# Kernel tuning notes

Measured on AMD Instinct MI355X. Metric: run time of the kernel, lower is better.

The kernel has to match this reference:

```python
import jax, jax.numpy as jnp
import numpy as np

# Config matching init_kwargs
D_MODEL = 1024   # input_size
D_HEAD = 2048    # head_size (expert hidden)
N_EXPERTS = 8
TOP_K = 2


def setup_inputs() -> dict:
    key = jax.random.key(0)
    k_x, k_g, k_w1, k_b1, k_w2, k_b2 = jax.random.split(key, 6)
    B, S = 4, 1024
    x = jax.random.normal(k_x, (B, S, D_MODEL), dtype=jnp.float32)
    # f_gate: nn.Linear(input_size, num_experts, bias=False) -> weight [E, D]
    gate_w = jax.random.normal(k_g, (N_EXPERTS, D_MODEL), dtype=jnp.float32) * 0.02
    # experts: ParallelExperts weights [E, in, out]
    s1 = 1.0 / D_MODEL
    s2 = 1.0 / D_HEAD
    w1 = jax.random.uniform(k_w1, (N_EXPERTS, D_MODEL, D_HEAD), jnp.float32, -s1, s1)
    b1 = jax.random.uniform(k_b1, (N_EXPERTS, D_HEAD), jnp.float32, -s1, s1)
    w2 = jax.random.uniform(k_w2, (N_EXPERTS, D_HEAD, D_MODEL), jnp.float32, -s2, s2)
    b2 = jax.random.uniform(k_b2, (N_EXPERTS, D_MODEL), jnp.float32, -s2, s2)
    return {"x": x, "gate_w": gate_w, "w1": w1, "b1": b1, "w2": w2, "b2": b2}


def reference(x, gate_w, w1, b1, w2, b2):
    B, S, D = x.shape
    xt = x.reshape(-1, D)                                   # [N, D]
    N = xt.shape[0]
    # --- gating (noisy_gating=False, eval path of top_k_gating) ---
    logits = xt @ gate_w.T                                  # [N, E]
    probs = jax.nn.softmax(logits, axis=-1)
    top_g, top_i = jax.lax.top_k(probs, TOP_K)              # [N, k]
    # gates = zeros.scatter(1, top_k_indices, top_k_gates)
    gates = jnp.zeros_like(probs).at[jnp.arange(N)[:, None], top_i].set(top_g)  # [N, E]
    # --- dispatch / grouped GEMM / combine ---
    # Equivalent dense-per-expert form: gates[n,e]==0 for non-routed tokens,
    # so y[n] = sum_e gates[n,e] * f_e(x[n]) exactly matches the
    # sort/scatter + per-expert torch.mm dispatch of ParallelLinear.
    y = jnp.zeros_like(xt)
    for e in range(N_EXPERTS):
        h = jax.nn.gelu(xt @ w1[e] + b1[e], approximate=False)  # [N, H]
        y = y + gates[:, e:e + 1] * (h @ w2[e] + b2[e])
    return y.reshape(B, S, D)
```

## Files before the change

kernel.cpp:

```cpp
#include <hip/hip_runtime.h>
#include <hip/hip_bf16.h>
#include <cstdint>
#include <cstddef>

#define N_TOK 4096
#define DM    1024
#define DH    2048
#define NE    8
#define BM    128
#define BN    128
#define BK    64
#define MAXT  80
#define TPX   (MAXT / 8)
#define HROWS (MAXT * BM)

typedef unsigned short u16t;
typedef __attribute__((ext_vector_type(4))) float          f32x4;
typedef __attribute__((ext_vector_type(8))) unsigned short u16x8;

__device__ __forceinline__ u16t f2b(float f) {
  union { float f; unsigned u; } v; v.f = f;
  return (u16t)((v.u + 0x7FFFu + ((v.u >> 16) & 1u)) >> 16);
}

__device__ __forceinline__ void gload16(const void* g, void* l) {
  auto gp = (const __attribute__((address_space(1))) unsigned int*)(uintptr_t)g;
  auto lp = (__attribute__((address_space(3))) unsigned int*)(uintptr_t)l;
  __builtin_amdgcn_global_load_lds(gp, lp, 16, 0, 0);
}

__device__ __forceinline__ void mfma16(f32x4& c, u16x8 a, u16x8 b) {
  asm("v_mfma_f32_16x16x32_bf16 %0, %1, %2, %0" : "+v"(c) : "v"(a), "v"(b));
}

__global__ void __launch_bounds__(256) k_prep(
    const float* __restrict__ x,  const float* __restrict__ gw,
    const float* __restrict__ w1, const float* __restrict__ w2,
    u16t* __restrict__ x16, u16t* __restrict__ w1t, u16t* __restrict__ w2t,
    int* __restrict__ topi, float* __restrict__ topg) {
  __shared__ float smem[NE * DM];
  int b = blockIdx.x;
  int tid = threadIdx.x;
  if (b < 8192) {
    const float* src; u16t* dst; int R, C, bx, by, bz;
    if (b < 4096) {
      int l = b; bz = l >> 9; int rem = l & 511;
      R = DM; C = DH; bx = rem & 31; by = rem >> 5; src = w1; dst = w1t;
    } else {
      int l = b - 4096; bz = l >> 9; int rem = l & 511;
      R = DH; C = DM; bx = rem & 15; by = rem >> 4; src = w2; dst = w2t;
    }
    float (*t)[65] = reinterpret_cast<float(*)[65]>(smem);
    const float* s = src + (size_t)bz * R * C;
    u16t* d = dst + (size_t)bz * R * C;
    int r0 = by * 64, c0 = bx * 64;
#pragma unroll
    for (int i = 0; i < 16; ++i) {
      int idx = i * 256 + tid;
      int r = idx >> 6, c = idx & 63;
      t[r][c] = s[(size_t)(r0 + r) * C + (c0 + c)];
    }
    __syncthreads();
#pragma unroll
    for (int i = 0; i < 16; ++i) {
      int idx = i * 256 + tid;
      int rr = idx >> 6, cc = idx & 63;
      d[(size_t)(c0 + rr) * R + (r0 + cc)] = f2b(t[cc][rr]);
    }
  } else {
    float* gws = smem;
#pragma unroll
    for (int i = 0; i < NE * DM / 256; ++i) gws[i * 256 + tid] = gw[i * 256 + tid];
    __syncthreads();
    int wv = tid >> 6, lane = tid & 63;
    int t = (b - 8192) * 4 + wv;
    float acc[NE];
#pragma unroll
    for (int e = 0; e < NE; ++e) acc[e] = 0.f;
    const float* xr = x + (size_t)t * DM;
    u16t* xo = x16 + (size_t)t * DM;
#pragma unroll
    for (int c = 0; c < DM / 64; ++c) {
      float xv = xr[c * 64 + lane];
      xo[c * 64 + lane] = f2b(xv);
#pragma unroll
      for (int e = 0; e < NE; ++e) acc[e] += xv * gws[e * DM + c * 64 + lane];
    }
#pragma unroll
    for (int e = 0; e < NE; ++e) {
#pragma unroll
      for (int m = 1; m < 64; m <<= 1) acc[e] += __shfl_xor(acc[e], m);
    }
    float mx = acc[0];
#pragma unroll
    for (int e = 1; e < NE; ++e) mx = fmaxf(mx, acc[e]);
    float p[NE], s = 0.f;
#pragma unroll
    for (int e = 0; e < NE; ++e) { p[e] = expf(acc[e] - mx); s += p[e]; }
    float inv = 1.f / s;
#pragma unroll
    for (int e = 0; e < NE; ++e) p[e] *= inv;
    int i1 = 0; float g1 = p[0];
#pragma unroll
    for (int e = 1; e < NE; ++e) if (p[e] > g1) { g1 = p[e]; i1 = e; }
    int i2 = -1; float g2 = -1.f;
#pragma unroll
    for (int e = 0; e < NE; ++e) if (e != i1 && p[e] > g2) { g2 = p[e]; i2 = e; }
    if (lane == 0) {
      topi[t * 2 + 0] = i1; topi[t * 2 + 1] = i2;
      topg[t * 2 + 0] = g1; topg[t * 2 + 1] = g2;
    }
  }
}

__global__ void __launch_bounds__(1024) k_scan(const int* __restrict__ topi,
                                               int* __restrict__ offe,
                                               int* __restrict__ cur64,
                                               int* __restrict__ te,
                                               int* __restrict__ trs,
                                               int* __restrict__ tnr,
                                               int* __restrict__ ntiles) {
  __shared__ int hist[NE];
  int tid = threadIdx.x;
  if (tid < NE) { hist[tid] = 0; cur64[tid * 16] = 0; }
  __syncthreads();
  int lc[NE];
#pragma unroll
  for (int e = 0; e < NE; ++e) lc[e] = 0;
#pragma unroll
  for (int i = 0; i < (N_TOK * 2) / 1024; ++i) {
    int v = topi[tid * ((N_TOK * 2) / 1024) + i];
#pragma unroll
    for (int e = 0; e < NE; ++e) lc[e] += (v == e);
  }
#pragma unroll
  for (int e = 0; e < NE; ++e) {
#pragma unroll
    for (int m = 1; m < 64; m <<= 1) lc[e] += __shfl_xor(lc[e], m);
  }
  if ((tid & 63) == 0) {
#pragma unroll
    for (int e = 0; e < NE; ++e) atomicAdd(&hist[e], lc[e]);
  }
  __syncthreads();
  if (tid == 0) {
    int off = 0, nt = 0;
    for (int e = 0; e < NE; ++e) {
      offe[e] = off;
      int c = hist[e];
      for (int i = 0; i < c; i += BM) {
        te[nt] = e; trs[nt] = off + i; tnr[nt] = min(BM, c - i); ++nt;
      }
      off += c;
    }
    *ntiles = nt;
  }
}

__global__ void k_scatter(const int* __restrict__ topi, const int* __restrict__ offe,
                          int* __restrict__ cur64, int* __restrict__ pair) {
  int t = blockIdx.x * blockDim.x + threadIdx.x;
  int lane = threadIdx.x & 63;
#pragma unroll
  for (int s = 0; s < 2; ++s) {
    int e = topi[t * 2 + s];
    int pos = 0;
#pragma unroll
    for (int ee = 0; ee < NE; ++ee) {
      unsigned long long mask = __ballot(e == ee);
      if (e == ee) {
        int rank = __popcll(mask & ((1ull << lane) - 1ull));
        int leader = __ffsll((long long)mask) - 1;
        int base = 0;
        if (lane == leader) base = atomicAdd(&cur64[ee * 16], (int)__popcll(mask));
        base = __shfl(base, leader);
        pos = offe[ee] + base + rank;
      }
    }
    pair[pos] = t * 2 + s;
  }
}

__global__ void __launch_bounds__(256, 2) k_gemm1(
    const u16t* __restrict__ x16, const u16t* __restrict__ w1t,
    const float* __restrict__ b1, u16t* __restrict__ h16,
    const int* __restrict__ pair, const int* __restrict__ te,
    const int* __restrict__ trs, const int* __restrict__ tnr,
    const int* __restrict__ ntiles) {
  int b = blockIdx.x;
  int ty = (b & 7) * TPX + ((b >> 3) % TPX);
  int n0 = ((b >> 3) / TPX) * BN;
  if (ty >= *ntiles) return;
  int e = te[ty], rs = trs[ty], nr = tnr[ty];
  __shared__ u16t As[BM * BK];
  __shared__ u16t Bs[BN * BK];
  __shared__ int tok[BM];
  int tid = threadIdx.x;
  if (tid < BM) {
    int p = rs + (tid < nr ? tid : nr - 1);
    tok[tid] = pair[p] >> 1;
  }
  __syncthreads();
  const u16t* aptr[4]; const u16t* bptr[4];
#pragma unroll
  for (int it = 0; it < 4; ++it) {
    int idx = it * 256 + tid;
    int r = idx >> 3, c = idx & 7;
    int cs = c ^ (r & 7);
    aptr[it] = x16 + (size_t)tok[r] * DM + cs * 8;
    bptr[it] = w1t + (size_t)e * DH * DM + (size_t)(n0 + r) * DM + cs * 8;
  }
  f32x4 acc[4][4];
#pragma unroll
  for (int m = 0; m < 4; ++m)
#pragma unroll
    for (int n = 0; n < 4; ++n) acc[m][n] = {0.f, 0.f, 0.f, 0.f};
  int lane = tid & 63, wv = tid >> 6;
  int wr = (wv >> 1) * 64, wc = (wv & 1) * 64;
  for (int k0 = 0; k0 < DM; k0 += BK) {
#pragma unroll
    for (int it = 0; it < 4; ++it) {
      int idx = it * 256 + tid;
      gload16(aptr[it] + k0, &As[idx * 8]);
      gload16(bptr[it] + k0, &Bs[idx * 8]);
    }
    __syncthreads();
#pragma unroll
    for (int kk = 0; kk < 2; ++kk) {
      u16x8 af[4], bf[4];
#pragma unroll
      for (int m = 0; m < 4; ++m) {
        int row = wr + m * 16 + (lane & 15);
        int cs = (kk * 4 + (lane >> 4)) ^ (row & 7);
        af[m] = *reinterpret_cast<const u16x8*>(&As[row * BK + cs * 8]);
      }
#pragma unroll
      for (int n = 0; n < 4; ++n) {
        int row = wc + n * 16 + (lane & 15);
        int cs = (kk * 4 + (lane >> 4)) ^ (row & 7);
        bf[n] = *reinterpret_cast<const u16x8*>(&Bs[row * BK + cs * 8]);
      }
#pragma unroll
      for (int m = 0; m < 4; ++m)
#pragma unroll
        for (int n = 0; n < 4; ++n) mfma16(acc[m][n], af[m], bf[n]);
    }
    __syncthreads();
  }
#pragma unroll
  for (int n = 0; n < 4; ++n) {
    int col = n0 + wc + n * 16 + (lane & 15);
    float bias = b1[e * DH + col];
#pragma unroll
    for (int m = 0; m < 4; ++m) {
#pragma unroll
      for (int r = 0; r < 4; ++r) {
        int rl = wr + m * 16 + ((lane >> 4) << 2) + r;
        if (rl < nr) {
          float z = acc[m][n][r] + bias;
          float g = 0.5f * z * (1.0f + erff(z * 0.70710678118654752440f));
          h16[(size_t)(rs + rl) * DH + col] = f2b(g);
        }
      }
    }
  }
}

__global__ void __launch_bounds__(256, 2) k_gemm2(
    const u16t* __restrict__ h16, const u16t* __restrict__ w2t,
    const float* __restrict__ b2, float* __restrict__ out,
    const int* __restrict__ pair, const float* __restrict__ topg,
    const int* __restrict__ te, const int* __restrict__ trs,
    const int* __restrict__ tnr, const int* __restrict__ ntiles) {
  int b = blockIdx.x;
  int ty = (b & 7) * TPX + ((b >> 3) % TPX);
  int n0 = ((b >> 3) / TPX) * BN;
  if (ty >= *ntiles) return;
  int e = te[ty], rs = trs[ty], nr = tnr[ty];
  __shared__ u16t As[BM * BK];
  __shared__ u16t Bs[BN * BK];
  __shared__ int tsl[BM];
  __shared__ float gl[BM];
  int tid = threadIdx.x;
  if (tid < BM) {
    int p = rs + (tid < nr ? tid : nr - 1);
    int ts = pair[p];
    tsl[tid] = ts;
    gl[tid] = topg[ts];
  }
  __syncthreads();
  const u16t* aptr[4]; const u16t* bptr[4];
#pragma unroll
  for (int it = 0; it < 4; ++it) {
    int idx = it * 256 + tid;
    int r = idx >> 3, c = idx & 7;
    int cs = c ^ (r & 7);
    aptr[it] = h16 + (size_t)(rs + r) * DH + cs * 8;
    bptr[it] = w2t + (size_t)e * DM * DH + (size_t)(n0 + r) * DH + cs * 8;
  }
  f32x4 acc[4][4];
#pragma unroll
  for (int m = 0; m < 4; ++m)
#pragma unroll
    for (int n = 0; n < 4; ++n) acc[m][n] = {0.f, 0.f, 0.f, 0.f};
  int lane = tid & 63, wv = tid >> 6;
  int wr = (wv >> 1) * 64, wc = (wv & 1) * 64;
  for (int k0 = 0; k0 < DH; k0 += BK) {
#pragma unroll
    for (int it = 0; it < 4; ++it) {
      int idx = it * 256 + tid;
      gload16(aptr[it] + k0, &As[idx * 8]);
      gload16(bptr[it] + k0, &Bs[idx * 8]);
    }
    __syncthreads();
#pragma unroll
    for (int kk = 0; kk < 2; ++kk) {
      u16x8 af[4], bf[4];
#pragma unroll
      for (int m = 0; m < 4; ++m) {
        int row = wr + m * 16 + (lane & 15);
        int cs = (kk * 4 + (lane >> 4)) ^ (row & 7);
        af[m] = *reinterpret_cast<const u16x8*>(&As[row * BK + cs * 8]);
      }
#pragma unroll
      for (int n = 0; n < 4; ++n) {
        int row = wc + n * 16 + (lane & 15);
        int cs = (kk * 4 + (lane >> 4)) ^ (row & 7);
        bf[n] = *reinterpret_cast<const u16x8*>(&Bs[row * BK + cs * 8]);
      }
#pragma unroll
      for (int m = 0; m < 4; ++m)
#pragma unroll
        for (int n = 0; n < 4; ++n) mfma16(acc[m][n], af[m], bf[n]);
    }
    __syncthreads();
  }
  float bias[4];
#pragma unroll
  for (int n = 0; n < 4; ++n) bias[n] = b2[e * DM + n0 + wc + n * 16 + (lane & 15)];
#pragma unroll
  for (int m = 0; m < 4; ++m) {
#pragma unroll
    for (int r = 0; r < 4; ++r) {
      int rl = wr + m * 16 + ((lane >> 4) << 2) + r;
      if (rl < nr) {
        int ts = tsl[rl];
        float g = gl[rl];
        float* orow = out + (size_t)(ts >> 1) * DM;
#pragma unroll
        for (int n = 0; n < 4; ++n) {
          int col = n0 + wc + n * 16 + (lane & 15);
          float v = g * (acc[m][n][r] + bias[n]);
          unsafeAtomicAdd(&orow[col], v);
        }
      }
    }
  }
}

extern "C" void kernel_launch(void* const* d_in, const int* in_sizes, int n_in,
                              void* d_out, int out_size, void* d_ws, size_t ws_size,
                              hipStream_t stream) {
  const float* x  = (const float*)d_in[0];
  const float* gw = (const float*)d_in[1];
  const float* w1 = (const float*)d_in[2];
  const float* b1 = (const float*)d_in[3];
  const float* w2 = (const float*)d_in[4];
  const float* b2 = (const float*)d_in[5];
  float* out = (float*)d_out;
  char* ws = (char*)d_ws;

  size_t o = 0;
  auto alloc = [&](size_t b) { size_t p = o; o += (b + 255) & ~(size_t)255; return p; };
  size_t X16  = alloc((size_t)N_TOK * DM * 2);
  size_t W1T  = alloc((size_t)NE * DH * DM * 2);
  size_t W2T  = alloc((size_t)NE * DM * DH * 2);
  size_t HB   = alloc((size_t)HROWS * DH * 2);
  size_t TOPI = alloc((size_t)N_TOK * 2 * 4);
  size_t TOPG = alloc((size_t)N_TOK * 2 * 4);
  size_t PAIR = alloc((size_t)HROWS * 4);
  size_t CUR  = alloc(NE * 64);
  size_t OFE  = alloc(64);
  size_t TE   = alloc(MAXT * 4);
  size_t TRS  = alloc(MAXT * 4);
  size_t TNR  = alloc(MAXT * 4);
  size_t NT   = alloc(64);
  (void)ws_size; (void)in_sizes; (void)n_in;

  hipMemsetAsync(out, 0, (size_t)out_size * 4, stream);

  k_prep<<<8192 + N_TOK / 4, 256, 0, stream>>>(
      x, gw, w1, w2, (u16t*)(ws + X16), (u16t*)(ws + W1T), (u16t*)(ws + W2T),
      (int*)(ws + TOPI), (float*)(ws + TOPG));
  k_scan<<<1, 1024, 0, stream>>>((int*)(ws + TOPI), (int*)(ws + OFE), (int*)(ws + CUR),
                                 (int*)(ws + TE), (int*)(ws + TRS), (int*)(ws + TNR),
                                 (int*)(ws + NT));
  k_scatter<<<N_TOK / 256, 256, 0, stream>>>((int*)(ws + TOPI), (int*)(ws + OFE),
                                             (int*)(ws + CUR), (int*)(ws + PAIR));
  k_gemm1<<<(DH / BN) * MAXT, 256, 0, stream>>>(
      (const u16t*)(ws + X16), (const u16t*)(ws + W1T), b1, (u16t*)(ws + HB),
      (const int*)(ws + PAIR), (const int*)(ws + TE), (const int*)(ws + TRS),
      (const int*)(ws + TNR), (const int*)(ws + NT));
  k_gemm2<<<(DM / BN) * MAXT, 256, 0, stream>>>(
      (const u16t*)(ws + HB), (const u16t*)(ws + W2T), b2, out,
      (const int*)(ws + PAIR), (const float*)(ws + TOPG), (const int*)(ws + TE),
      (const int*)(ws + TRS), (const int*)(ws + TNR), (const int*)(ws + NT));
}
```

Baseline: 200.3 us.

## Widen grouped GEMM tiles to 128x256 with 512-thread blocks and dynamic tile mapping

Measured after the change: 204.2 us. About the same (+1.9%).

```diff
diff --git a/kernel.cpp b/kernel.cpp
--- a/kernel.cpp
+++ b/kernel.cpp
@@ -8,10 +8,11 @@
 #define DH    2048
 #define NE    8
 #define BM    128
-#define BN    128
+#define BN1   256
+#define BN2   256
 #define BK    64
 #define MAXT  80
-#define TPX   (MAXT / 8)
+#define TPXM  ((MAXT + 7) / 8)
 #define HROWS (MAXT * BM)
 
 typedef unsigned short u16t;
@@ -181,19 +182,23 @@
   }
 }
 
-__global__ void __launch_bounds__(256, 2) k_gemm1(
+__global__ void __launch_bounds__(512, 4) k_gemm1(
     const u16t* __restrict__ x16, const u16t* __restrict__ w1t,
     const float* __restrict__ b1, u16t* __restrict__ h16,
     const int* __restrict__ pair, const int* __restrict__ te,
     const int* __restrict__ trs, const int* __restrict__ tnr,
     const int* __restrict__ ntiles) {
+  int nt = *ntiles;
   int b = blockIdx.x;
-  int ty = (b & 7) * TPX + ((b >> 3) % TPX);
-  int n0 = ((b >> 3) / TPX) * BN;
-  if (ty >= *ntiles) return;
+  int xcd = b & 7, elem = b >> 3;
+  int tpx = (nt + 7) >> 3;
+  if (elem >= tpx * (DH / BN1)) return;
+  int ty = xcd * tpx + (elem % tpx);
+  if (ty >= nt) return;
+  int n0 = (elem / tpx) * BN1;
   int e = te[ty], rs = trs[ty], nr = tnr[ty];
   __shared__ u16t As[BM * BK];
-  __shared__ u16t Bs[BN * BK];
+  __shared__ u16t Bs[BN1 * BK];
   __shared__ int tok[BM];
   int tid = threadIdx.x;
   if (tid < BM) {
@@ -201,13 +206,19 @@
     tok[tid] = pair[p] >> 1;
   }
   __syncthreads();
-  const u16t* aptr[4]; const u16t* bptr[4];
-#pragma unroll
-  for (int it = 0; it < 4; ++it) {
-    int idx = it * 256 + tid;
+  const u16t* aptr[2]; const u16t* bptr[4];
+#pragma unroll
+  for (int it = 0; it < 2; ++it) {
+    int idx = it * 512 + tid;
     int r = idx >> 3, c = idx & 7;
     int cs = c ^ (r & 7);
     aptr[it] = x16 + (size_t)tok[r] * DM + cs * 8;
+  }
+#pragma unroll
+  for (int it = 0; it < 4; ++it) {
+    int idx = it * 512 + tid;
+    int r = idx >> 3, c = idx & 7;
+    int cs = c ^ (r & 7);
     bptr[it] = w1t + (size_t)e * DH * DM + (size_t)(n0 + r) * DM + cs * 8;
   }
   f32x4 acc[4][4];
@@ -216,12 +227,16 @@
 #pragma unroll
     for (int n = 0; n < 4; ++n) acc[m][n] = {0.f, 0.f, 0.f, 0.f};
   int lane = tid & 63, wv = tid >> 6;
-  int wr = (wv >> 1) * 64, wc = (wv & 1) * 64;
+  int wr = (wv >> 2) * 64, wc = (wv & 3) * 64;
   for (int k0 = 0; k0 < DM; k0 += BK) {
 #pragma unroll
+    for (int it = 0; it < 2; ++it) {
+      int idx = it * 512 + tid;
+      gload16(aptr[it] + k0, &As[idx * 8]);
+    }
+#pragma unroll
     for (int it = 0; it < 4; ++it) {
-      int idx = it * 256 + tid;
-      gload16(aptr[it] + k0, &As[idx * 8]);
+      int idx = it * 512 + tid;
       gload16(bptr[it] + k0, &Bs[idx * 8]);
     }
     __syncthreads();
@@ -266,19 +281,23 @@
   }
 }
 
-__global__ void __launch_bounds__(256, 2) k_gemm2(
+__global__ void __launch_bounds__(512, 4) k_gemm2(
     const u16t* __restrict__ h16, const u16t* __restrict__ w2t,
     const float* __restrict__ b2, float* __restrict__ out,
     const int* __restrict__ pair, const float* __restrict__ topg,
     const int* __restrict__ te, const int* __restrict__ trs,
     const int* __restrict__ tnr, const int* __restrict__ ntiles) {
+  int nt = *ntiles;
   int b = blockIdx.x;
-  int ty = (b & 7) * TPX + ((b >> 3) % TPX);
-  int n0 = ((b >> 3) / TPX) * BN;
-  if (ty >= *ntiles) return;
+  int xcd = b & 7, elem = b >> 3;
+  int tpx = (nt + 7) >> 3;
+  if (elem >= tpx * (DM / BN2)) return;
+  int ty = xcd * tpx + (elem % tpx);
+  if (ty >= nt) return;
+  int n0 = (elem / tpx) * BN2;
   int e = te[ty], rs = trs[ty], nr = tnr[ty];
   __shared__ u16t As[BM * BK];
-  __shared__ u16t Bs[BN * BK];
+  __shared__ u16t Bs[BN2 * BK];
   __shared__ int tsl[BM];
   __shared__ float gl[BM];
   int tid = threadIdx.x;
@@ -289,13 +308,19 @@
     gl[tid] = topg[ts];
   }
   __syncthreads();
-  const u16t* aptr[4]; const u16t* bptr[4];
-#pragma unroll
-  for (int it = 0; it < 4; ++it) {
-    int idx = it * 256 + tid;
+  const u16t* aptr[2]; const u16t* bptr[4];
+#pragma unroll
+  for (int it = 0; it < 2; ++it) {
+    int idx = it * 512 + tid;
     int r = idx >> 3, c = idx & 7;
     int cs = c ^ (r & 7);
     aptr[it] = h16 + (size_t)(rs + r) * DH + cs * 8;
+  }
+#pragma unroll
+  for (int it = 0; it < 4; ++it) {
+    int idx = it * 512 + tid;
+    int r = idx >> 3, c = idx & 7;
+    int cs = c ^ (r & 7);
     bptr[it] = w2t + (size_t)e * DM * DH + (size_t)(n0 + r) * DH + cs * 8;
   }
   f32x4 acc[4][4];
@@ -304,12 +329,16 @@
 #pragma unroll
     for (int n = 0; n < 4; ++n) acc[m][n] = {0.f, 0.f, 0.f, 0.f};
   int lane = tid & 63, wv = tid >> 6;
-  int wr = (wv >> 1) * 64, wc = (wv & 1) * 64;
+  int wr = (wv >> 2) * 64, wc = (wv & 3) * 64;
   for (int k0 = 0; k0 < DH; k0 += BK) {
 #pragma unroll
+    for (int it = 0; it < 2; ++it) {
+      int idx = it * 512 + tid;
+      gload16(aptr[it] + k0, &As[idx * 8]);
+    }
+#pragma unroll
     for (int it = 0; it < 4; ++it) {
-      int idx = it * 256 + tid;
-      gload16(aptr[it] + k0, &As[idx * 8]);
+      int idx = it * 512 + tid;
       gload16(bptr[it] + k0, &Bs[idx * 8]);
     }
     __syncthreads();
@@ -397,11 +426,11 @@
                                  (int*)(ws + NT));
   k_scatter<<<N_TOK / 256, 256, 0, stream>>>((int*)(ws + TOPI), (int*)(ws + OFE),
                                              (int*)(ws + CUR), (int*)(ws + PAIR));
-  k_gemm1<<<(DH / BN) * MAXT, 256, 0, stream>>>(
+  k_gemm1<<<8 * TPXM * (DH / BN1), 512, 0, stream>>>(
       (const u16t*)(ws + X16), (const u16t*)(ws + W1T), b1, (u16t*)(ws + HB),
       (const int*)(ws + PAIR), (const int*)(ws + TE), (const int*)(ws + TRS),
       (const int*)(ws + TNR), (const int*)(ws + NT));
-  k_gemm2<<<(DM / BN) * MAXT, 256, 0, stream>>>(
+  k_gemm2<<<8 * TPXM * (DM / BN2), 512, 0, stream>>>(
       (const u16t*)(ws + HB), (const u16t*)(ws + W2T), b2, out,
       (const int*)(ws + PAIR), (const float*)(ws + TOPG), (const int*)(ws + TE),
       (const int*)(ws + TRS), (const int*)(ws + TNR), (const int*)(ws + NT));
```
